# Kernel optimization log

Hardware: AMD Instinct MI355X
Metric: run time of the kernel (lower is better)

## Reference

```python
import jax, jax.numpy as jnp
import numpy as np

FP8 = jnp.float8_e4m3fn

def setup_inputs() -> dict:
    key = jax.random.key(0)
    k_in, k_w = jax.random.split(key)
    M, H = 16384, 4096
    input = jax.random.normal(k_in, (M, H), dtype=jnp.float32)
    # learned fp8 weight, materialized as float32 then quantized in reference
    weight = jax.random.normal(k_w, (H, H), dtype=jnp.float32) * 0.02
    scale_b = jnp.ones((1, H), dtype=jnp.float32)  # per-column dequant scale
    return {"input": input, "weight": weight, "scale_b": scale_b, "world_size": 8}

def reference(input, weight, scale_b, world_size):
    # fp8 quantize input and weight (torch._scaled_mm consumes fp8 operands)
    a = input.astype(FP8).astype(jnp.float32)            # [M, H]
    b = weight.astype(FP8).astype(jnp.float32)           # [H, H]
    scale_a = jnp.ones((input.shape[0], 1), dtype=jnp.float32)  # [M, 1]
    # scaled_mm: (a @ b) * scale_a * scale_b, out_dtype=fp16
    out = (a @ b) * scale_a * scale_b                    # [M, H] fp32 accumulate
    out = out.astype(jnp.float16)
    # reduce_scatter along dim 0: sum corresponding shards across world_size ranks
    M, H = out.shape
    rs = out.reshape(world_size, M // world_size, H).sum(axis=0)  # [M/world, H]
    return rs.astype(jnp.float16)
```

## Files before the change

kernel.cpp:

```cpp
#include <hip/hip_runtime.h>

#define MFULL 16384
#define MOUT  2048
#define H     4096
#define WS    8

typedef _Float16 f16x8 __attribute__((ext_vector_type(8)));
typedef _Float16 f16x4 __attribute__((ext_vector_type(4)));
typedef _Float16 f16x2 __attribute__((ext_vector_type(2)));
typedef float    f32x4 __attribute__((ext_vector_type(4)));
typedef float    f32x2 __attribute__((ext_vector_type(2)));

__device__ __forceinline__ void fp8_rt4(float4& v) {
    int p0 = __builtin_amdgcn_cvt_pk_fp8_f32(v.x, v.y, 0, false);
    int p1 = __builtin_amdgcn_cvt_pk_fp8_f32(v.z, v.w, 0, false);
    f32x2 r0 = __builtin_amdgcn_cvt_pk_f32_fp8(p0, false);
    f32x2 r1 = __builtin_amdgcn_cvt_pk_f32_fp8(p1, false);
    v.x = r0.x; v.y = r0.y; v.z = r1.x; v.w = r1.y;
}

__device__ __forceinline__ float fp8_rt1(float x) {
    int p = __builtin_amdgcn_cvt_pk_fp8_f32(x, x, 0, false);
    return __builtin_amdgcn_cvt_f32_fp8(p, 0);
}

__device__ __forceinline__ void async_copy16(const void* g, void* l) {
    __builtin_amdgcn_global_load_lds(
        (const __attribute__((address_space(1))) void*)g,
        (__attribute__((address_space(3))) void*)l, 16, 0, 0);
}

__global__ void reduce_quant_a(const float* __restrict__ in,
                               _Float16* __restrict__ aq) {
    int idx = blockIdx.x * 256 + threadIdx.x;
    int r = idx >> 10;
    int k = (idx & 1023) * 4;
    const float* p = in + (size_t)r * H + k;
    float4 acc = {0.f, 0.f, 0.f, 0.f};
#pragma unroll
    for (int s = 0; s < WS; ++s) {
        float4 v = *(const float4*)(p + (size_t)s * MOUT * H);
        fp8_rt4(v);
        acc.x += v.x; acc.y += v.y; acc.z += v.z; acc.w += v.w;
    }
    f16x4 h = { (_Float16)acc.x, (_Float16)acc.y, (_Float16)acc.z, (_Float16)acc.w };
    *(f16x4*)(aq + (size_t)r * H + k) = h;
}

__global__ void quant_transpose_b(const float* __restrict__ w,
                                  _Float16* __restrict__ bt) {
    __shared__ _Float16 tile[64][66];
    int t  = threadIdx.x;
    int n0 = blockIdx.x * 64;
    int k0 = blockIdx.y * 64;
#pragma unroll
    for (int i = 0; i < 16; ++i) {
        int lin = i * 256 + t;
        int kl = lin >> 6;
        int nl = lin & 63;
        float v = w[(size_t)(k0 + kl) * H + n0 + nl];
        tile[kl][nl] = (_Float16)fp8_rt1(v);
    }
    __syncthreads();
#pragma unroll
    for (int i = 0; i < 8; ++i) {
        int lin = i * 256 + t;
        int kl = (lin & 31) * 2;
        int nl = lin >> 5;
        f16x2 hv = { tile[kl][nl], tile[kl + 1][nl] };
        *(f16x2*)(bt + (size_t)(n0 + nl) * H + k0 + kl) = hv;
    }
}

__global__ __launch_bounds__(256) void gemm_rs(
    const _Float16* __restrict__ A, const _Float16* __restrict__ Bt,
    const float* __restrict__ scale_b, float* __restrict__ out) {
    __shared__ _Float16 As[128 * 32];
    __shared__ _Float16 Bs[128 * 32];

    const int tid  = threadIdx.x;
    const int wid  = tid >> 6;
    const int lane = tid & 63;
    const int quad = lane >> 4;
    const int l16  = lane & 15;
    const int bm   = blockIdx.y * 128;
    const int bn   = blockIdx.x * 128;
    const int wm   = (wid >> 1) * 64;
    const int wn   = (wid & 1) * 64;

    f32x4 acc[4][4] = {};

    const _Float16* Ab = A  + (size_t)bm * H;
    const _Float16* Bb = Bt + (size_t)bn * H;

    int chunk0 = wid * 64 + lane;
    int row0 = chunk0 >> 2, s0 = chunk0 & 3;
    int kc0 = s0 ^ ((row0 >> 2) & 3);
    int chunk1 = (4 + wid) * 64 + lane;
    int row1 = chunk1 >> 2, s1 = chunk1 & 3;
    int kc1 = s1 ^ ((row1 >> 2) & 3);

    const size_t ga0 = (size_t)row0 * H + kc0 * 8;
    const size_t ga1 = (size_t)row1 * H + kc1 * 8;
    char* la0 = (char*)As + wid * 1024;
    char* la1 = (char*)As + (4 + wid) * 1024;
    char* lb0 = (char*)Bs + wid * 1024;
    char* lb1 = (char*)Bs + (4 + wid) * 1024;

    const int fslot = quad ^ (l16 >> 2);
    const int foff  = fslot * 8;

    for (int k0 = 0; k0 < H; k0 += 32) {
        async_copy16(Ab + ga0 + k0, la0);
        async_copy16(Ab + ga1 + k0, la1);
        async_copy16(Bb + ga0 + k0, lb0);
        async_copy16(Bb + ga1 + k0, lb1);
        __syncthreads();

        f16x8 af[4], bf[4];
#pragma unroll
        for (int i = 0; i < 4; ++i)
            af[i] = *(const f16x8*)&As[(wm + i * 16 + l16) * 32 + foff];
#pragma unroll
        for (int i = 0; i < 4; ++i)
            bf[i] = *(const f16x8*)&Bs[(wn + i * 16 + l16) * 32 + foff];
#pragma unroll
        for (int i = 0; i < 4; ++i)
#pragma unroll
            for (int j = 0; j < 4; ++j)
                acc[i][j] = __builtin_amdgcn_mfma_f32_16x16x32_f16(
                    af[i], bf[j], acc[i][j], 0, 0, 0);
        __syncthreads();
    }

#pragma unroll
    for (int i = 0; i < 4; ++i) {
#pragma unroll
        for (int j = 0; j < 4; ++j) {
            int col = bn + wn + j * 16 + l16;
            float sb = scale_b[col];
#pragma unroll
            for (int r = 0; r < 4; ++r) {
                int row = bm + wm + i * 16 + quad * 4 + r;
                float v = acc[i][j][r] * sb;
                out[(size_t)row * H + col] = (float)(_Float16)v;
            }
        }
    }
}

extern "C" void kernel_launch(void* const* d_in, const int* in_sizes, int n_in,
                              void* d_out, int out_size, void* d_ws, size_t ws_size,
                              hipStream_t stream) {
    const float* input   = (const float*)d_in[0];
    const float* weight  = (const float*)d_in[1];
    const float* scale_b = (const float*)d_in[2];
    float* out = (float*)d_out;

    _Float16* aq = (_Float16*)d_ws;
    _Float16* bt = aq + (size_t)MOUT * H;

    reduce_quant_a<<<(MOUT * H / 4) / 256, 256, 0, stream>>>(input, aq);
    quant_transpose_b<<<dim3(H / 64, H / 64), 256, 0, stream>>>(weight, bt);
    gemm_rs<<<dim3(H / 128, MOUT / 128), 256, 0, stream>>>(aq, bt, scale_b, out);
}
```

Measured before the change: 509.6 us.

## Split GEMM K dimension in two and add a reduction/scale kernel

The GEMM grid gains a K-split dimension of 2, so each block accumulates half of K and writes fp32 partials to a workspace buffer. A new kernel sums the two partials, applies the per-column scale and rounds to fp16. This doubles the block count from 512 to 1024 to fill the GPU's compute units better. In exchange it adds 64 MB of partial-sum traffic and an extra kernel launch.

Result: slower. 538.5 us (+5.7%).

```diff
diff --git a/kernel.cpp b/kernel.cpp
--- a/kernel.cpp
+++ b/kernel.cpp
@@ -4,6 +4,8 @@
 #define MOUT  2048
 #define H     4096
 #define WS    8
+#define KSPLIT 2
+#define KHALF (H / KSPLIT)
 
 typedef _Float16 f16x8 __attribute__((ext_vector_type(8)));
 typedef _Float16 f16x4 __attribute__((ext_vector_type(4)));
@@ -72,9 +74,9 @@
     }
 }
 
-__global__ __launch_bounds__(256) void gemm_rs(
+__global__ __launch_bounds__(256) void gemm_splitk(
     const _Float16* __restrict__ A, const _Float16* __restrict__ Bt,
-    const float* __restrict__ scale_b, float* __restrict__ out) {
+    float* __restrict__ P) {
     __shared__ _Float16 As[128 * 32];
     __shared__ _Float16 Bs[128 * 32];
 
@@ -85,13 +87,14 @@
     const int l16  = lane & 15;
     const int bm   = blockIdx.y * 128;
     const int bn   = blockIdx.x * 128;
+    const int koff = blockIdx.z * KHALF;
     const int wm   = (wid >> 1) * 64;
     const int wn   = (wid & 1) * 64;
 
     f32x4 acc[4][4] = {};
 
-    const _Float16* Ab = A  + (size_t)bm * H;
-    const _Float16* Bb = Bt + (size_t)bn * H;
+    const _Float16* Ab = A  + (size_t)bm * H + koff;
+    const _Float16* Bb = Bt + (size_t)bn * H + koff;
 
     int chunk0 = wid * 64 + lane;
     int row0 = chunk0 >> 2, s0 = chunk0 & 3;
@@ -110,7 +113,7 @@
     const int fslot = quad ^ (l16 >> 2);
     const int foff  = fslot * 8;
 
-    for (int k0 = 0; k0 < H; k0 += 32) {
+    for (int k0 = 0; k0 < KHALF; k0 += 32) {
         async_copy16(Ab + ga0 + k0, la0);
         async_copy16(Ab + ga1 + k0, la1);
         async_copy16(Bb + ga0 + k0, lb0);
@@ -133,20 +136,35 @@
         __syncthreads();
     }
 
+    float* Pz = P + (size_t)blockIdx.z * MOUT * H;
 #pragma unroll
     for (int i = 0; i < 4; ++i) {
 #pragma unroll
         for (int j = 0; j < 4; ++j) {
             int col = bn + wn + j * 16 + l16;
-            float sb = scale_b[col];
 #pragma unroll
             for (int r = 0; r < 4; ++r) {
                 int row = bm + wm + i * 16 + quad * 4 + r;
-                float v = acc[i][j][r] * sb;
-                out[(size_t)row * H + col] = (float)(_Float16)v;
+                Pz[(size_t)row * H + col] = acc[i][j][r];
             }
         }
     }
+}
+
+__global__ void reduce_scale(const float* __restrict__ P,
+                             const float* __restrict__ scale_b,
+                             float* __restrict__ out) {
+    int idx = blockIdx.x * 256 + threadIdx.x;
+    int c4 = (idx & (H / 4 - 1)) * 4;
+    float4 p0 = ((const float4*)P)[idx];
+    float4 p1 = ((const float4*)(P + (size_t)MOUT * H))[idx];
+    float4 sb = *(const float4*)(scale_b + c4);
+    float4 r;
+    r.x = (float)(_Float16)((p0.x + p1.x) * sb.x);
+    r.y = (float)(_Float16)((p0.y + p1.y) * sb.y);
+    r.z = (float)(_Float16)((p0.z + p1.z) * sb.z);
+    r.w = (float)(_Float16)((p0.w + p1.w) * sb.w);
+    ((float4*)out)[idx] = r;
 }
 
 extern "C" void kernel_launch(void* const* d_in, const int* in_sizes, int n_in,
@@ -159,8 +177,10 @@
 
     _Float16* aq = (_Float16*)d_ws;
     _Float16* bt = aq + (size_t)MOUT * H;
+    float*    P  = (float*)(bt + (size_t)H * H);
 
     reduce_quant_a<<<(MOUT * H / 4) / 256, 256, 0, stream>>>(input, aq);
     quant_transpose_b<<<dim3(H / 64, H / 64), 256, 0, stream>>>(weight, bt);
-    gemm_rs<<<dim3(H / 128, MOUT / 128), 256, 0, stream>>>(aq, bt, scale_b, out);
+    gemm_splitk<<<dim3(H / 128, MOUT / 128, KSPLIT), 256, 0, stream>>>(aq, bt, P);
+    reduce_scale<<<(MOUT * H / 4) / 256, 256, 0, stream>>>(P, scale_b, out);
 }
```
